# Kernel optimization log

Measured on AMD Instinct MI355X. Metric: run time of the kernel, lower is better.

## Reference

```python
import jax, jax.numpy as jnp
import numpy as np

N = 10000
E = 160000
D_IN = 512
D_HID = 512


def gcn_conv(x, W, b, src, dst, norm, num_nodes):
    # x: [N, Fin] -> h: [N, Fout]; PyG GCNConv: linear transform, then
    # symmetric-normalized aggregation over edges with self-loops.
    h = x @ W + b  # [N, Fout]
    msgs = h[src] * norm[:, None]  # [E', Fout]
    return jax.ops.segment_sum(msgs, dst, num_segments=num_nodes)


def _norm_with_self_loops(edge_index, num_nodes):
    loop = jnp.arange(num_nodes, dtype=edge_index.dtype)
    src = jnp.concatenate([edge_index[0], loop])
    dst = jnp.concatenate([edge_index[1], loop])
    deg = jax.ops.segment_sum(jnp.ones_like(dst, dtype=jnp.float32), dst,
                              num_segments=num_nodes)
    dis = jnp.where(deg > 0, jax.lax.rsqrt(jnp.maximum(deg, 1.0)), 0.0)
    norm = dis[src] * dis[dst]
    return src, dst, norm


def setup_inputs() -> dict:
    key = jax.random.key(0)
    ks = jax.random.split(key, 8)
    x = jax.random.normal(ks[0], (N, D_IN), dtype=jnp.float32)
    edge_index = jax.random.randint(ks[1], (2, E), 0, N, dtype=jnp.int64)
    s1 = 1.0 / np.sqrt(D_IN)
    s2 = 1.0 / np.sqrt(D_HID)
    W1 = jax.random.uniform(ks[2], (D_IN, D_HID), jnp.float32, -s1, s1)
    b1 = jnp.zeros((D_HID,), jnp.float32)
    W2 = jax.random.uniform(ks[3], (D_HID, D_IN), jnp.float32, -s2, s2)
    b2 = jnp.zeros((D_IN,), jnp.float32)
    Wp1 = jax.random.uniform(ks[4], (D_HID, D_HID), jnp.float32, -s2, s2)
    bp1 = jnp.zeros((D_HID,), jnp.float32)
    Wp2 = jax.random.uniform(ks[5], (D_HID, D_HID), jnp.float32, -s2, s2)
    bp2 = jnp.zeros((D_HID,), jnp.float32)
    return {"x": x, "edge_index": edge_index, "W1": W1, "b1": b1,
            "W2": W2, "b2": b2, "Wp1": Wp1, "bp1": bp1,
            "Wp2": Wp2, "bp2": bp2}


def reference(x, edge_index, W1, b1, W2, b2, Wp1, bp1, Wp2, bp2):
    num_nodes = x.shape[0]
    src, dst, norm = _norm_with_self_loops(edge_index, num_nodes)
    z = gcn_conv(x, W1, b1, src, dst, norm, num_nodes)        # [N, hidden]
    h = jax.nn.relu(z)
    out = gcn_conv(h, W2, b2, src, dst, norm, num_nodes)      # [N, in]
    proj = jax.nn.relu(z @ Wp1 + bp1) @ Wp2 + bp2             # [N, hidden]
    return (out, z, proj)
```

## Files before the change

kernel.cpp:

```cpp
#include <hip/hip_runtime.h>
#include <stddef.h>

#define N_NODES 10000
#define N_EDGES 160000
#define DIM     512
#define RBT     158
#define RB128   79
#define GBLKS   (RB128 * 4)
#define SCAN_BLKS 40
#define EBLKS   625

typedef short bf16x8 __attribute__((ext_vector_type(8)));
typedef float f32x4  __attribute__((ext_vector_type(4)));

__device__ inline unsigned short bf16_rne(float f) {
    unsigned u = __builtin_bit_cast(unsigned, f);
    u += 0x7FFF + ((u >> 16) & 1);
    return (unsigned short)(u >> 16);
}
__device__ inline float bf16_to_f32(unsigned short h) {
    unsigned u = ((unsigned)h) << 16;
    return __builtin_bit_cast(float, u);
}

__device__ inline void gld_lds16(const void* g, void* lds) {
    __builtin_amdgcn_global_load_lds(
        (const __attribute__((address_space(1))) void*)g,
        (__attribute__((address_space(3))) void*)lds, 16, 0, 0);
}


__global__ __launch_bounds__(256) void packw_zero_kernel(
    const float* __restrict__ W1, const float* __restrict__ W2,
    const float* __restrict__ Wp1, const float* __restrict__ Wp2,
    short* __restrict__ T1, short* __restrict__ T2,
    short* __restrict__ Tp1, short* __restrict__ Tp2,
    int* __restrict__ deg) {
    const int bid = blockIdx.x;
    if (bid >= 512) {
        int i = (bid - 512) * 256 + threadIdx.x;
        if (i < N_NODES) deg[i] = 0;
        return;
    }
    const int wsel = bid >> 7;
    const float* W = (wsel == 0) ? W1 : (wsel == 1) ? W2 : (wsel == 2) ? Wp1 : Wp2;
    short* WT      = (wsel == 0) ? T1 : (wsel == 1) ? T2 : (wsel == 2) ? Tp1 : Tp2;
    int id = (bid & 127) * 256 + threadIdx.x;
    int n  = id & 511;
    int kc = id >> 9;
    int colblk = n >> 6, col = n & 63;
    int kt = kc >> 2, kq = kc & 3;
    short hi[8];
#pragma unroll
    for (int j = 0; j < 8; ++j)
        hi[j] = (short)bf16_rne(W[(size_t)(kc * 8 + j) * 512 + n]);
    size_t base = (size_t)(colblk * 16 + kt) * 2048 + col * 32 + ((kq ^ ((col >> 1) & 3)) << 3);
    *(int4*)(WT + base) = *(const int4*)hi;
}


__global__ __launch_bounds__(256) void packa_count_kernel(
    const float* __restrict__ A, short* __restrict__ P0,
    const int* __restrict__ ei, int* __restrict__ deg) {
    const int bid = blockIdx.x;
    if (bid >= RBT * 16) {
        int e = (bid - RBT * 16) * 256 + threadIdx.x;
        if (e < N_EDGES) atomicAdd(&deg[ei[N_EDGES + e]], 1);
        return;
    }
    const int kt = bid & 15;
    const int rb = bid >> 4;
    const int t  = threadIdx.x;
    const int r  = t >> 2;
    const int kq = t & 3;
    const int row = rb * 64 + r;
    float v[8] = {};
    if (row < N_NODES) {
        float4 a = *(const float4*)(A + (size_t)row * 512 + kt * 32 + kq * 8);
        float4 b = *(const float4*)(A + (size_t)row * 512 + kt * 32 + kq * 8 + 4);
        v[0]=a.x; v[1]=a.y; v[2]=a.z; v[3]=a.w; v[4]=b.x; v[5]=b.y; v[6]=b.z; v[7]=b.w;
    }
    short hi[8];
#pragma unroll
    for (int j = 0; j < 8; ++j) hi[j] = (short)bf16_rne(v[j]);
    size_t base = (size_t)(rb * 16 + kt) * 2048 + r * 32 + ((kq ^ ((r >> 1) & 3)) << 3);
    *(int4*)(P0 + base) = *(const int4*)hi;
}


__global__ __launch_bounds__(256) void scan1_kernel(const int* __restrict__ deg,
                                                    int* __restrict__ row_off,
                                                    int* __restrict__ bsum,
                                                    float* __restrict__ dis,
                                                    int* __restrict__ cursor, int n) {
    __shared__ int sm[256];
    const int i = blockIdx.x * 256 + threadIdx.x;
    int v = (i < n) ? deg[i] : 0;
    if (i < n) {
        dis[i] = rsqrtf((float)(v + 1));
        cursor[i] = 0;
    }
    sm[threadIdx.x] = v;
    __syncthreads();
    for (int off = 1; off < 256; off <<= 1) {
        int t = (threadIdx.x >= (unsigned)off) ? sm[threadIdx.x - off] : 0;
        __syncthreads();
        sm[threadIdx.x] += t;
        __syncthreads();
    }
    if (i < n) row_off[i + 1] = sm[threadIdx.x];
    if (threadIdx.x == 255) bsum[blockIdx.x] = sm[255];
}

__global__ __launch_bounds__(64) void scan2_kernel(int* __restrict__ bsum) {
    const int lane = threadIdx.x;
    int v0 = (lane < SCAN_BLKS) ? bsum[lane] : 0;
    int v = v0;
    for (int off = 1; off < 64; off <<= 1) {
        int t = __shfl_up(v, off, 64);
        if (lane >= off) v += t;
    }
    if (lane < SCAN_BLKS) bsum[lane] = v - v0;
}

__global__ __launch_bounds__(256) void scan3_kernel(int* __restrict__ row_off,
                                                    const int* __restrict__ bsum, int n) {
    const int i = blockIdx.x * 256 + threadIdx.x;
    if (i < n) row_off[i + 1] += bsum[blockIdx.x];
    if (i == 0) row_off[0] = 0;
}


__device__ __forceinline__ void map_block(int bid, int& rb, int& cb) {
    const int q = GBLKS / 8;
    const int r = GBLKS % 8;
    int xcd = bid & 7;
    int idx = bid >> 3;
    int L = (xcd < r ? xcd * (q + 1) : r * (q + 1) + (xcd - r) * q) + idx;
    cb = L / RB128;
    rb = L - cb * RB128;
}

__device__ __forceinline__ void gemm128_core(
    const short* __restrict__ Apk, const short* __restrict__ Wpk,
    int bid, f32x4 (&acc)[4][4],
    short (*As)[4096], short (*Bs)[4096],
    int& rb, int& cb, int& wr, int& wc)
{
    map_block(bid, rb, cb);
    const int tid = threadIdx.x;
    const int w = tid >> 6;
    wr = w >> 1;
    wc = w & 1;
    const int lane = tid & 63;
    const int l15 = lane & 15, kg = lane >> 4;
    const int kso = ((kg ^ ((l15 >> 1) & 3)) << 3);
    const int wofs = w * 1024;

    const char* At0 = (const char*)(Apk + (size_t)(rb * 2)     * 16 * 2048);
    const char* At1 = (const char*)(Apk + (size_t)(rb * 2 + 1) * 16 * 2048);
    const char* Bt0 = (const char*)(Wpk + (size_t)(cb * 2)     * 16 * 2048);
    const char* Bt1 = (const char*)(Wpk + (size_t)(cb * 2 + 1) * 16 * 2048);

#pragma unroll
    for (int i = 0; i < 4; ++i)
#pragma unroll
        for (int j = 0; j < 4; ++j) acc[i][j] = (f32x4){0.f, 0.f, 0.f, 0.f};

    auto stage = [&](int buf, int kt) {
        const int go = kt * 4096 + tid * 16;
        char* ad = (char*)&As[buf][0];
        char* bd = (char*)&Bs[buf][0];
        gld_lds16(At0 + go, ad + wofs);
        gld_lds16(At1 + go, ad + 4096 + wofs);
        gld_lds16(Bt0 + go, bd + wofs);
        gld_lds16(Bt1 + go, bd + 4096 + wofs);
    };

    stage(0, 0);
    __syncthreads();

#pragma unroll
    for (int kt = 0; kt < 16; ++kt) {
        const int buf = kt & 1;
        if (kt < 15) stage(buf ^ 1, kt + 1);

        const short* as = &As[buf][wr * 2048];
        const short* bs = &Bs[buf][wc * 2048];
        bf16x8 af[4], bf[4];
#pragma unroll
        for (int m = 0; m < 4; ++m)
            af[m] = *(const bf16x8*)&as[(m * 16 + l15) * 32 + kso];
#pragma unroll
        for (int n = 0; n < 4; ++n)
            bf[n] = *(const bf16x8*)&bs[(n * 16 + l15) * 32 + kso];
#pragma unroll
        for (int m = 0; m < 4; ++m)
#pragma unroll
            for (int n = 0; n < 4; ++n)
                acc[m][n] = __builtin_amdgcn_mfma_f32_16x16x32_bf16(af[m], bf[n], acc[m][n], 0, 0, 0);
        __syncthreads();
    }
}


template<bool RELU_OUT>
__device__ __forceinline__ void epi128_f32(f32x4 (&acc)[4][4], const float* bias,
                                           float* C, int rb, int cb, int wr, int wc) {
    const int lane = threadIdx.x & 63;
    const int l15 = lane & 15, kg = lane >> 4;
#pragma unroll
    for (int n = 0; n < 4; ++n) {
        int c = cb * 128 + wc * 64 + n * 16 + l15;
        float bv = bias[c];
#pragma unroll
        for (int m = 0; m < 4; ++m) {
            int r0 = rb * 128 + wr * 64 + m * 16 + kg * 4;
#pragma unroll
            for (int j = 0; j < 4; ++j) {
                int row = r0 + j;
                if (row < N_NODES) {
                    float v = acc[m][n][j] + bv;
                    if (RELU_OUT) v = fmaxf(v, 0.f);
                    C[(size_t)row * 512 + c] = v;
                }
            }
        }
    }
}

__device__ __forceinline__ void epi128_bf16(f32x4 (&acc)[4][4], const float* bias,
                                            unsigned short* C, int rb, int cb, int wr, int wc) {
    const int lane = threadIdx.x & 63;
    const int l15 = lane & 15, kg = lane >> 4;
#pragma unroll
    for (int n = 0; n < 4; ++n) {
        int c = cb * 128 + wc * 64 + n * 16 + l15;
        float bv = bias[c];
#pragma unroll
        for (int m = 0; m < 4; ++m) {
            int r0 = rb * 128 + wr * 64 + m * 16 + kg * 4;
#pragma unroll
            for (int j = 0; j < 4; ++j) {
                int row = r0 + j;
                if (row < N_NODES)
                    C[(size_t)row * 512 + c] = bf16_rne(acc[m][n][j] + bv);
            }
        }
    }
}

__device__ __forceinline__ void epi128_pack(f32x4 (&acc)[4][4], const float* bias,
                                            short* Cpk, int rb, int cb, int wr, int wc) {
    const int lane = threadIdx.x & 63;
    const int l15 = lane & 15, kg = lane >> 4;
#pragma unroll
    for (int n = 0; n < 4; ++n) {
        int c = cb * 128 + wc * 64 + n * 16 + l15;
        int kt_n = c >> 5, kk = c & 31, kgn = kk >> 3, kj = kk & 7;
        float bv = bias[c];
#pragma unroll
        for (int m = 0; m < 4; ++m) {
#pragma unroll
            for (int j = 0; j < 4; ++j) {
                int grow = rb * 128 + wr * 64 + m * 16 + kg * 4 + j;
                float v = (grow < N_NODES) ? fmaxf(acc[m][n][j] + bv, 0.f) : 0.f;
                int rt = grow >> 6, rl = grow & 63;
                size_t dst = (size_t)(rt * 16 + kt_n) * 2048 + rl * 32
                           + ((kgn ^ ((rl >> 1) & 3)) << 3) + kj;
                Cpk[dst] = (short)bf16_rne(v);
            }
        }
    }
}


__global__ __launch_bounds__(256, 4) void gemm1_scatter_kernel(
    const short* __restrict__ APKx, const short* __restrict__ WT1,
    const float* __restrict__ b1, unsigned short* __restrict__ Hb,
    const int* __restrict__ ei, const float* __restrict__ dis,
    const int* __restrict__ row_off, int* __restrict__ cursor,
    int* __restrict__ csr_src, float* __restrict__ csr_norm)
{
    __shared__ short As[2][4096];
    __shared__ short Bs[2][4096];
    const int bid = blockIdx.x;
    if (bid >= GBLKS) {
        int e = (bid - GBLKS) * 256 + threadIdx.x;
        if (e < N_EDGES) {
            int s = ei[e];
            int d = ei[N_EDGES + e];
            int slot = row_off[d] + atomicAdd(&cursor[d], 1);
            csr_src[slot]  = s;
            csr_norm[slot] = dis[s] * dis[d];
        }
        return;
    }
    f32x4 acc[4][4];
    int rb, cb, wr, wc;
    gemm128_core(APKx, WT1, bid, acc, As, Bs, rb, cb, wr, wc);
    epi128_bf16(acc, b1, Hb, rb, cb, wr, wc);
}


__global__ __launch_bounds__(256) void agg1_pack_kernel(
    const unsigned short* __restrict__ Hb,
    const float* __restrict__ dis,
    const int* __restrict__ row_off,
    const int* __restrict__ csr_src,
    const float* __restrict__ csr_norm,
    float* __restrict__ z,
    short* __restrict__ ZPKp, short* __restrict__ ZPKr)
{
    const int node = blockIdx.x;
    const int t = threadIdx.x;
    const int f0 = 2 * t;
    const int kt = f0 >> 5, kq = (f0 >> 3) & 3, j = f0 & 7;
    const int rb = node >> 6, r = node & 63;
    const size_t dst = (size_t)(rb * 16 + kt) * 2048 + r * 32 + ((kq ^ ((r >> 1) & 3)) << 3) + j;

    if (node >= N_NODES) {
        ushort2 zz = make_ushort2(0, 0);
        *(ushort2*)(ZPKp + dst) = zz;
        *(ushort2*)(ZPKr + dst) = zz;
        return;
    }

    const int start = row_off[node];
    const int end   = row_off[node + 1];
    const float dn = dis[node];
    const float sw = dn * dn;

    ushort2 hv = *((const ushort2*)(Hb + (size_t)node * DIM) + t);
    float a0 = bf16_to_f32(hv.x) * sw;
    float a1 = bf16_to_f32(hv.y) * sw;

    int e = start;
    for (; e + 3 < end; e += 4) {
        int s0 = csr_src[e],     s1 = csr_src[e + 1];
        int s2 = csr_src[e + 2], s3 = csr_src[e + 3];
        float w0 = csr_norm[e],     w1 = csr_norm[e + 1];
        float w2 = csr_norm[e + 2], w3 = csr_norm[e + 3];
        ushort2 v0 = *((const ushort2*)(Hb + (size_t)s0 * DIM) + t);
        ushort2 v1 = *((const ushort2*)(Hb + (size_t)s1 * DIM) + t);
        ushort2 v2 = *((const ushort2*)(Hb + (size_t)s2 * DIM) + t);
        ushort2 v3 = *((const ushort2*)(Hb + (size_t)s3 * DIM) + t);
        a0 += bf16_to_f32(v0.x) * w0 + bf16_to_f32(v1.x) * w1
            + bf16_to_f32(v2.x) * w2 + bf16_to_f32(v3.x) * w3;
        a1 += bf16_to_f32(v0.y) * w0 + bf16_to_f32(v1.y) * w1
            + bf16_to_f32(v2.y) * w2 + bf16_to_f32(v3.y) * w3;
    }
    for (; e < end; ++e) {
        int s = csr_src[e];
        float w = csr_norm[e];
        ushort2 v = *((const ushort2*)(Hb + (size_t)s * DIM) + t);
        a0 += bf16_to_f32(v.x) * w;
        a1 += bf16_to_f32(v.y) * w;
    }
    *((float2*)(z + (size_t)node * DIM) + t) = make_float2(a0, a1);

    *(ushort2*)(ZPKp + dst) = make_ushort2(bf16_rne(a0), bf16_rne(a1));
    *(ushort2*)(ZPKr + dst) = make_ushort2(bf16_rne(fmaxf(a0, 0.f)), bf16_rne(fmaxf(a1, 0.f)));
}


__global__ __launch_bounds__(256, 4) void gemm23_kernel(
    const short* __restrict__ ZPKr, const short* __restrict__ WT2,
    const float* __restrict__ b2, unsigned short* __restrict__ Hb,
    const short* __restrict__ ZPKp, const short* __restrict__ WTp1,
    const float* __restrict__ bp1, short* __restrict__ APKp1)
{
    __shared__ short As[2][4096];
    __shared__ short Bs[2][4096];
    const int bid = blockIdx.x;
    f32x4 acc[4][4];
    int rb, cb, wr, wc;
    if (bid < GBLKS) {
        gemm128_core(ZPKr, WT2, bid, acc, As, Bs, rb, cb, wr, wc);
        epi128_bf16(acc, b2, Hb, rb, cb, wr, wc);
    } else {
        gemm128_core(ZPKp, WTp1, bid - GBLKS, acc, As, Bs, rb, cb, wr, wc);
        epi128_pack(acc, bp1, APKp1, rb, cb, wr, wc);
    }
}


__global__ __launch_bounds__(256) void agg2_kernel(
    const unsigned short* __restrict__ Hb, const float* __restrict__ dis,
    const int* __restrict__ row_off, const int* __restrict__ csr_src,
    const float* __restrict__ csr_norm, float* __restrict__ out)
{
    const int node = blockIdx.x;
    const int t = threadIdx.x;
    const int start = row_off[node];
    const int end   = row_off[node + 1];
    const float dn = dis[node];
    const float sw = dn * dn;

    ushort2 hv = *((const ushort2*)(Hb + (size_t)node * DIM) + t);
    float a0 = bf16_to_f32(hv.x) * sw;
    float a1 = bf16_to_f32(hv.y) * sw;

    int e = start;
    for (; e + 3 < end; e += 4) {
        int s0 = csr_src[e],     s1 = csr_src[e + 1];
        int s2 = csr_src[e + 2], s3 = csr_src[e + 3];
        float w0 = csr_norm[e],     w1 = csr_norm[e + 1];
        float w2 = csr_norm[e + 2], w3 = csr_norm[e + 3];
        ushort2 v0 = *((const ushort2*)(Hb + (size_t)s0 * DIM) + t);
        ushort2 v1 = *((const ushort2*)(Hb + (size_t)s1 * DIM) + t);
        ushort2 v2 = *((const ushort2*)(Hb + (size_t)s2 * DIM) + t);
        ushort2 v3 = *((const ushort2*)(Hb + (size_t)s3 * DIM) + t);
        a0 += bf16_to_f32(v0.x) * w0 + bf16_to_f32(v1.x) * w1
            + bf16_to_f32(v2.x) * w2 + bf16_to_f32(v3.x) * w3;
        a1 += bf16_to_f32(v0.y) * w0 + bf16_to_f32(v1.y) * w1
            + bf16_to_f32(v2.y) * w2 + bf16_to_f32(v3.y) * w3;
    }
    for (; e < end; ++e) {
        int s = csr_src[e];
        float w = csr_norm[e];
        ushort2 v = *((const ushort2*)(Hb + (size_t)s * DIM) + t);
        a0 += bf16_to_f32(v.x) * w;
        a1 += bf16_to_f32(v.y) * w;
    }
    *((float2*)(out + (size_t)node * DIM) + t) = make_float2(a0, a1);
}


__global__ __launch_bounds__(256, 4) void gemm4_kernel(
    const short* __restrict__ APKp1, const short* __restrict__ WTp2,
    const float* __restrict__ bp2, float* __restrict__ proj)
{
    __shared__ short As[2][4096];
    __shared__ short Bs[2][4096];
    f32x4 acc[4][4];
    int rb, cb, wr, wc;
    gemm128_core(APKp1, WTp2, blockIdx.x, acc, As, Bs, rb, cb, wr, wc);
    epi128_f32<false>(acc, bp2, proj, rb, cb, wr, wc);
}


extern "C" void kernel_launch(void* const* d_in, const int* in_sizes, int n_in,
                              void* d_out, int out_size, void* d_ws, size_t ws_size,
                              hipStream_t stream) {
    const float* x   = (const float*)d_in[0];
    const int*   ei  = (const int*)d_in[1];
    const float* W1  = (const float*)d_in[2];
    const float* b1  = (const float*)d_in[3];
    const float* W2  = (const float*)d_in[4];
    const float* b2  = (const float*)d_in[5];
    const float* Wp1 = (const float*)d_in[6];
    const float* bp1 = (const float*)d_in[7];
    const float* Wp2 = (const float*)d_in[8];
    const float* bp2 = (const float*)d_in[9];

    float* out  = (float*)d_out;
    float* z    = out + (size_t)N_NODES * DIM;
    float* proj = z   + (size_t)N_NODES * DIM;

    char* ws = (char*)d_ws;
    size_t off = 0;
    auto walloc = [&](size_t bytes) -> void* {
        void* p = ws + off;
        off = (off + bytes + 255) & ~(size_t)255;
        return p;
    };
    const size_t PK_SHORTS = (size_t)RBT * 16 * 2048;
    unsigned short* Hb = (unsigned short*)walloc((size_t)N_NODES * DIM * sizeof(unsigned short));
    short* APKx  = (short*)walloc(PK_SHORTS * sizeof(short));
    short* ZPKp  = (short*)walloc(PK_SHORTS * sizeof(short));
    short* ZPKr  = (short*)walloc(PK_SHORTS * sizeof(short));
    short* APKp1 = (short*)walloc(PK_SHORTS * sizeof(short));
    short* WT1  = (short*)walloc((size_t)8 * 16 * 2048 * sizeof(short));
    short* WT2  = (short*)walloc((size_t)8 * 16 * 2048 * sizeof(short));
    short* WTp1 = (short*)walloc((size_t)8 * 16 * 2048 * sizeof(short));
    short* WTp2 = (short*)walloc((size_t)8 * 16 * 2048 * sizeof(short));
    int*   deg      = (int*)  walloc(N_NODES * sizeof(int));
    int*   cursor   = (int*)  walloc(N_NODES * sizeof(int));
    int*   row_off  = (int*)  walloc((N_NODES + 1) * sizeof(int));
    int*   bsum     = (int*)  walloc(SCAN_BLKS * sizeof(int));
    float* dis      = (float*)walloc(N_NODES * sizeof(float));
    int*   csr_src  = (int*)  walloc(N_EDGES * sizeof(int));
    float* csr_norm = (float*)walloc(N_EDGES * sizeof(float));

    const dim3 blk(256);
    const dim3 wave(64);

    packw_zero_kernel<<<dim3(512 + SCAN_BLKS), blk, 0, stream>>>(
        W1, W2, Wp1, Wp2, WT1, WT2, WTp1, WTp2, deg);
    packa_count_kernel<<<dim3(RBT * 16 + EBLKS), blk, 0, stream>>>(x, APKx, ei, deg);
    scan1_kernel<<<dim3(SCAN_BLKS), blk, 0, stream>>>(deg, row_off, bsum, dis, cursor, N_NODES);
    scan2_kernel<<<dim3(1), wave, 0, stream>>>(bsum);
    scan3_kernel<<<dim3(SCAN_BLKS), blk, 0, stream>>>(row_off, bsum, N_NODES);

    gemm1_scatter_kernel<<<dim3(GBLKS + EBLKS), blk, 0, stream>>>(
        APKx, WT1, b1, Hb, ei, dis, row_off, cursor, csr_src, csr_norm);
    agg1_pack_kernel<<<dim3(RB128 * 128), blk, 0, stream>>>(
        Hb, dis, row_off, csr_src, csr_norm, z, ZPKp, ZPKr);
    gemm23_kernel<<<dim3(2 * GBLKS), blk, 0, stream>>>(
        ZPKr, WT2, b2, Hb, ZPKp, WTp1, bp1, APKp1);
    agg2_kernel<<<dim3(N_NODES), blk, 0, stream>>>(Hb, dis, row_off, csr_src, csr_norm, out);
    gemm4_kernel<<<dim3(GBLKS), blk, 0, stream>>>(APKp1, WTp2, bp2, proj);
}
```

Before: 168.6 us.

## Share A tile between the W2 and Wp1 GEMMs and apply ReLU in-register

The two GEMMs that consume z now run in one 512-thread block that loads the z tile into LDS once and feeds it to two wave groups, one multiplying by W2 and one by Wp1. ReLU is applied to the bf16 fragments in registers for the W2 path, so agg1 no longer writes a separate ReLU'd packed copy of z. This removes one packed activation write and one A-tile read, at the cost of larger blocks, more LDS per block, and half as many blocks in the launch.

```diff
diff --git a/kernel.cpp b/kernel.cpp
--- a/kernel.cpp
+++ b/kernel.cpp
@@ -27,6 +27,13 @@
     __builtin_amdgcn_global_load_lds(
         (const __attribute__((address_space(1))) void*)g,
         (__attribute__((address_space(3))) void*)lds, 16, 0, 0);
+}
+
+__device__ __forceinline__ bf16x8 relu_pk(bf16x8 v) {
+    bf16x8 r;
+#pragma unroll
+    for (int i = 0; i < 8; ++i) r[i] = (v[i] < (short)0) ? (short)0 : v[i];
+    return r;
 }
 
 
@@ -310,7 +317,7 @@
     const int* __restrict__ csr_src,
     const float* __restrict__ csr_norm,
     float* __restrict__ z,
-    short* __restrict__ ZPKp, short* __restrict__ ZPKr)
+    short* __restrict__ ZPKp)
 {
     const int node = blockIdx.x;
     const int t = threadIdx.x;
@@ -320,9 +327,7 @@
     const size_t dst = (size_t)(rb * 16 + kt) * 2048 + r * 32 + ((kq ^ ((r >> 1) & 3)) << 3) + j;
 
     if (node >= N_NODES) {
-        ushort2 zz = make_ushort2(0, 0);
-        *(ushort2*)(ZPKp + dst) = zz;
-        *(ushort2*)(ZPKr + dst) = zz;
+        *(ushort2*)(ZPKp + dst) = make_ushort2(0, 0);
         return;
     }
 
@@ -358,30 +363,88 @@
         a1 += bf16_to_f32(v.y) * w;
     }
     *((float2*)(z + (size_t)node * DIM) + t) = make_float2(a0, a1);
-
     *(ushort2*)(ZPKp + dst) = make_ushort2(bf16_rne(a0), bf16_rne(a1));
-    *(ushort2*)(ZPKr + dst) = make_ushort2(bf16_rne(fmaxf(a0, 0.f)), bf16_rne(fmaxf(a1, 0.f)));
-}
-
-
-__global__ __launch_bounds__(256, 4) void gemm23_kernel(
-    const short* __restrict__ ZPKr, const short* __restrict__ WT2,
-    const float* __restrict__ b2, unsigned short* __restrict__ Hb,
-    const short* __restrict__ ZPKp, const short* __restrict__ WTp1,
-    const float* __restrict__ bp1, short* __restrict__ APKp1)
+}
+
+
+__global__ __launch_bounds__(512, 4) void gemm23_kernel(
+    const short* __restrict__ ZPKp,
+    const short* __restrict__ WT2,  const float* __restrict__ b2,
+    unsigned short* __restrict__ Hb,
+    const short* __restrict__ WTp1, const float* __restrict__ bp1,
+    short* __restrict__ APKp1)
 {
-    __shared__ short As[2][4096];
-    __shared__ short Bs[2][4096];
-    const int bid = blockIdx.x;
+    __shared__ short As [2][4096];
+    __shared__ short Bs2[2][4096];
+    __shared__ short Bsp[2][4096];
+
+    int rb, cb;
+    map_block(blockIdx.x, rb, cb);
+    const int tid = threadIdx.x;
+    const int w = tid >> 6;
+    const int g = w >> 2;
+    const int sub = w & 3;
+    const int wr = sub >> 1, wc = sub & 1;
+    const int lane = tid & 63;
+    const int l15 = lane & 15, kg = lane >> 4;
+    const int kso = ((kg ^ ((l15 >> 1) & 3)) << 3);
+
+    const char* Asrc[2] = {
+        (const char*)(ZPKp + (size_t)(rb * 2)     * 16 * 2048),
+        (const char*)(ZPKp + (size_t)(rb * 2 + 1) * 16 * 2048) };
+    const char* B2src[2] = {
+        (const char*)(WT2 + (size_t)(cb * 2)     * 16 * 2048),
+        (const char*)(WT2 + (size_t)(cb * 2 + 1) * 16 * 2048) };
+    const char* Bpsrc[2] = {
+        (const char*)(WTp1 + (size_t)(cb * 2)     * 16 * 2048),
+        (const char*)(WTp1 + (size_t)(cb * 2 + 1) * 16 * 2048) };
+
+    const int half = w >> 2;
+    const int sof  = (w & 3) * 1024 + lane * 16;
+    const int dof  = w * 1024;
+
     f32x4 acc[4][4];
-    int rb, cb, wr, wc;
-    if (bid < GBLKS) {
-        gemm128_core(ZPKr, WT2, bid, acc, As, Bs, rb, cb, wr, wc);
-        epi128_bf16(acc, b2, Hb, rb, cb, wr, wc);
-    } else {
-        gemm128_core(ZPKp, WTp1, bid - GBLKS, acc, As, Bs, rb, cb, wr, wc);
-        epi128_pack(acc, bp1, APKp1, rb, cb, wr, wc);
-    }
+#pragma unroll
+    for (int i = 0; i < 4; ++i)
+#pragma unroll
+        for (int j = 0; j < 4; ++j) acc[i][j] = (f32x4){0.f, 0.f, 0.f, 0.f};
+
+    auto stage = [&](int buf, int kt) {
+        const int so = kt * 4096 + sof;
+        gld_lds16(Asrc[half]  + so, (char*)&As [buf][0] + dof);
+        gld_lds16(B2src[half] + so, (char*)&Bs2[buf][0] + dof);
+        gld_lds16(Bpsrc[half] + so, (char*)&Bsp[buf][0] + dof);
+    };
+
+    stage(0, 0);
+    __syncthreads();
+
+#pragma unroll
+    for (int kt = 0; kt < 16; ++kt) {
+        const int buf = kt & 1;
+        if (kt < 15) stage(buf ^ 1, kt + 1);
+
+        const short* as = &As[buf][wr * 2048];
+        const short* bs = (g == 0) ? &Bs2[buf][wc * 2048] : &Bsp[buf][wc * 2048];
+        bf16x8 af[4], bf[4];
+#pragma unroll
+        for (int m = 0; m < 4; ++m) {
+            af[m] = *(const bf16x8*)&as[(m * 16 + l15) * 32 + kso];
+            if (g == 0) af[m] = relu_pk(af[m]);
+        }
+#pragma unroll
+        for (int n = 0; n < 4; ++n)
+            bf[n] = *(const bf16x8*)&bs[(n * 16 + l15) * 32 + kso];
+#pragma unroll
+        for (int m = 0; m < 4; ++m)
+#pragma unroll
+            for (int n = 0; n < 4; ++n)
+                acc[m][n] = __builtin_amdgcn_mfma_f32_16x16x32_bf16(af[m], bf[n], acc[m][n], 0, 0, 0);
+        __syncthreads();
+    }
+
+    if (g == 0) epi128_bf16(acc, b2, Hb, rb, cb, wr, wc);
+    else        epi128_pack(acc, bp1, APKp1, rb, cb, wr, wc);
 }
 
 
@@ -469,7 +532,6 @@
     unsigned short* Hb = (unsigned short*)walloc((size_t)N_NODES * DIM * sizeof(unsigned short));
     short* APKx  = (short*)walloc(PK_SHORTS * sizeof(short));
     short* ZPKp  = (short*)walloc(PK_SHORTS * sizeof(short));
-    short* ZPKr  = (short*)walloc(PK_SHORTS * sizeof(short));
     short* APKp1 = (short*)walloc(PK_SHORTS * sizeof(short));
     short* WT1  = (short*)walloc((size_t)8 * 16 * 2048 * sizeof(short));
     short* WT2  = (short*)walloc((size_t)8 * 16 * 2048 * sizeof(short));
@@ -496,9 +558,9 @@
     gemm1_scatter_kernel<<<dim3(GBLKS + EBLKS), blk, 0, stream>>>(
         APKx, WT1, b1, Hb, ei, dis, row_off, cursor, csr_src, csr_norm);
     agg1_pack_kernel<<<dim3(RB128 * 128), blk, 0, stream>>>(
-        Hb, dis, row_off, csr_src, csr_norm, z, ZPKp, ZPKr);
-    gemm23_kernel<<<dim3(2 * GBLKS), blk, 0, stream>>>(
-        ZPKr, WT2, b2, Hb, ZPKp, WTp1, bp1, APKp1);
+        Hb, dis, row_off, csr_src, csr_norm, z, ZPKp);
+    gemm23_kernel<<<dim3(GBLKS), dim3(512), 0, stream>>>(
+        ZPKp, WT2, b2, Hb, WTp1, bp1, APKp1);
     agg2_kernel<<<dim3(N_NODES), blk, 0, stream>>>(Hb, dis, row_off, csr_src, csr_norm, out);
     gemm4_kernel<<<dim3(GBLKS), blk, 0, stream>>>(APKp1, WTp2, bp2, proj);
 }
```

Result: slower. 172.6 us (+2.3%).
